# Kernel tuning notes

Measured on AMD Instinct MI355X. Metric: run time of the kernel, lower is better.

The kernel has to match this reference:

```python
import jax, jax.numpy as jnp
import numpy as np

BITS = (2, 4, 8)
GROUP = 4
EPS = 1e-5


def _ste_round(x):
    return x + jax.lax.stop_gradient(jnp.round(x) - x)


def _quant_act(x, b):
    s = float(2 ** b - 1)
    return _ste_round(jnp.clip(x, 0.0, 1.0) * s) / s


def _quant_weight(w, mean, std, b):
    # normalize by (mean, std) of the gating-selected channels, then b-bit uniform quant on [-1, 1]
    wn = jnp.clip((w - mean) / (std + EPS), -1.0, 1.0)
    s = float(2 ** b - 1)
    u = _ste_round((wn + 1.0) * 0.5 * s) / s
    return 2.0 * u - 1.0


def _mixed_qconv(x, w, w_mean, w_std, w_logits, a_logits):
    # bitwidth-selectable conv: softmax mixture over quantized weights / activations
    pw = jax.nn.softmax(w_logits)
    pa = jax.nn.softmax(a_logits)
    w_mix = sum(pw[i] * _quant_weight(w, w_mean, w_std, b) for i, b in enumerate(BITS))
    x_mix = sum(pa[i] * _quant_act(x, b) for i, b in enumerate(BITS))
    return jax.lax.conv_general_dilated(
        x_mix, w_mix, window_strides=(1, 1), padding='SAME',
        dimension_numbers=('NCHW', 'OIHW', 'NCHW'))


def _bn(x, g, b, m, v):
    inv = jax.lax.rsqrt(v + EPS)
    return (x - m[None, :, None, None]) * (g * inv)[None, :, None, None] + b[None, :, None, None]


def _masked_mean_std(w, mask):
    # mean/std over gate-selected filter slices; torch uses .data -> stop_gradient, unbiased std
    m = jnp.broadcast_to(mask, w.shape)
    cnt = jnp.sum(m)
    mean = jnp.sum(w * m) / cnt
    var = jnp.sum(m * (w - mean) ** 2) / (cnt - 1.0)
    return jax.lax.stop_gradient(mean), jax.lax.stop_gradient(jnp.sqrt(var))


def _indicator(w1, thr):
    n, c, h, wk = w1.shape
    fw = w1.reshape(n // GROUP, GROUP * c * h * wk)
    nf = fw / jnp.max(jnp.abs(fw))
    norm = jnp.sum(jnp.abs(nf), axis=1) / (GROUP * c * h * wk)  # [n_choices]
    soft = jax.nn.sigmoid(norm - thr)
    hard = (norm > thr).astype(w1.dtype)
    return hard - jax.lax.stop_gradient(soft) + soft  # STE indicator


def setup_inputs() -> dict:
    key = jax.random.key(0)
    ks = jax.random.split(key, 10)
    B, C, H, W = 64, 256, 32, 32
    return {
        'x': jax.random.normal(ks[0], (B, C, H, W), jnp.float32),
        'w1': jax.random.normal(ks[1], (C, C, 3, 3), jnp.float32) * 0.05,
        'w2': jax.random.normal(ks[2], (C, C, 3, 3), jnp.float32) * 0.05,
        'bn1_gamma': jnp.ones((C,), jnp.float32),
        'bn1_beta': jnp.zeros((C,), jnp.float32),
        'bn1_mean': jax.random.normal(ks[3], (C,), jnp.float32) * 0.1,
        'bn1_var': jax.random.uniform(ks[4], (C,), jnp.float32, 0.5, 1.5),
        'bn2_gamma': jnp.ones((C,), jnp.float32),
        'bn2_beta': jnp.zeros((C,), jnp.float32),
        'bn2_mean': jax.random.normal(ks[5], (C,), jnp.float32) * 0.1,
        'bn2_var': jax.random.uniform(ks[6], (C,), jnp.float32, 0.5, 1.5),
        'threshold': jnp.zeros((1,), jnp.float32),
        'w_logits1': jax.random.normal(ks[7], (3,), jnp.float32) * 0.1,
        'a_logits1': jax.random.normal(ks[8], (3,), jnp.float32) * 0.1,
        'w_logits2': jax.random.normal(ks[9], (3,), jnp.float32) * 0.1,
        'a_logits2': jnp.zeros((3,), jnp.float32),
    }


def reference(x, w1, w2, bn1_gamma, bn1_beta, bn1_mean, bn1_var,
              bn2_gamma, bn2_beta, bn2_mean, bn2_var, threshold,
              w_logits1, a_logits1, w_logits2, a_logits2):
    thr = threshold[0]
    ind = _indicator(w1, thr)                       # [n_choices]
    ind_ch = jnp.repeat(ind, GROUP)                 # [out_plane]
    gate_mask = jax.lax.stop_gradient((ind_ch > 0).astype(x.dtype))

    # both_preact path
    residual = x
    h = jax.nn.relu(_bn(x, bn1_gamma, bn1_beta, bn1_mean, bn1_var))
    m1, s1 = _masked_mean_std(w1, gate_mask[:, None, None, None])
    h = _mixed_qconv(h, w1, m1, s1, w_logits1, a_logits1)
    h = jax.nn.relu(_bn(h, bn2_gamma, bn2_beta, bn2_mean, bn2_var))
    m2, s2 = _masked_mean_std(w2, gate_mask[None, :, None, None])
    h = h * ind_ch[None, :, None, None]             # differentiable channel gating
    h = _mixed_qconv(h, w2, m2, s2, w_logits2, a_logits2)
    return h + residual
```

## Files before the change

kernel.cpp:

```cpp
#include <hip/hip_runtime.h>
#include <stdint.h>

#define EPSF 1e-5f

typedef _Float16 h8_t __attribute__((ext_vector_type(8)));
typedef float f4_t __attribute__((ext_vector_type(4)));

#define BB 64
#define CC 256
#define HH 32
#define WW 32
#define HP 34
#define WP 34
#define PADIMG (HP*WP*CC)
#define PADTOT (BB*PADIMG)

#define S_GSUM   0
#define S_GMAX   64
#define S_W1S    128
#define S_W1Q    192
#define S_W2S    256
#define S_W2Q    320
#define S_PA2    384
#define S_INDCH  400
#define S_BN2SC  656
#define S_BN2SH  912

#define OFF_STATS 0
#define OFF_A1    8192
#define OFF_A2    (OFF_A1 + PADTOT*2)
#define OFF_W1T   (OFF_A2 + PADTOT*2)
#define OFF_W2T   (OFF_W1T + 9*CC*CC*2)

__device__ __forceinline__ void async_load16(void* lds, const void* g) {
  __builtin_amdgcn_global_load_lds(
      reinterpret_cast<uint32_t __attribute__((address_space(1)))*>((uintptr_t)g),
      reinterpret_cast<uint32_t __attribute__((address_space(3)))*>((uint32_t)(uintptr_t)lds),
      16, 0, 0);
}

__device__ __forceinline__ float wave_sum(float v) {
  for (int o = 32; o; o >>= 1) v += __shfl_down(v, o);
  return v;
}
__device__ __forceinline__ float wave_max(float v) {
  for (int o = 32; o; o >>= 1) v = fmaxf(v, __shfl_down(v, o));
  return v;
}

__device__ __forceinline__ void softmax3(const float* l, float* out) {
  float m = fmaxf(fmaxf(l[0], l[1]), l[2]);
  float e0 = expf(l[0] - m), e1 = expf(l[1] - m), e2 = expf(l[2] - m);
  float inv = 1.f / (e0 + e1 + e2);
  out[0] = e0 * inv; out[1] = e1 * inv; out[2] = e2 * inv;
}

__device__ __forceinline__ float qmix_act(float v, float p0, float p1, float p2) {
  float cl = fminf(fmaxf(v, 0.f), 1.f);
  return p0 * (rintf(cl * 3.f) / 3.f) + p1 * (rintf(cl * 15.f) / 15.f)
       + p2 * (rintf(cl * 255.f) / 255.f);
}

__global__ void k_stats(const float* __restrict__ w1, const float* __restrict__ w2,
                        float* stats) {
  __shared__ float red[4][4];
  int bid = blockIdx.x, t = threadIdx.x;
  int lane = t & 63, w = t >> 6;
  if (bid < 64) {
    const float* p = w1 + bid * 9216;
    float sa = 0.f, s = 0.f, q = 0.f, mx = 0.f;
    for (int i = t; i < 9216; i += 256) {
      float v = p[i];
      float a = fabsf(v);
      sa += a; s += v; q += v * v; mx = fmaxf(mx, a);
    }
    sa = wave_sum(sa); s = wave_sum(s); q = wave_sum(q); mx = wave_max(mx);
    if (lane == 0) { red[w][0] = sa; red[w][1] = s; red[w][2] = q; red[w][3] = mx; }
    __syncthreads();
    if (t == 0) {
      float a = 0, b = 0, c = 0, d = 0;
      for (int k = 0; k < 4; ++k) {
        a += red[k][0]; b += red[k][1]; c += red[k][2]; d = fmaxf(d, red[k][3]);
      }
      stats[S_GSUM + bid] = a;
      stats[S_W1S + bid] = b;
      stats[S_W1Q + bid] = c;
      stats[S_GMAX + bid] = d;
    }
  } else {
    int g = bid - 64;
    const float* p = w2 + (size_t)t * 2304 + g * 36;
    float s = 0.f, q = 0.f;
#pragma unroll
    for (int i = 0; i < 36; ++i) { float v = p[i]; s += v; q += v * v; }
    s = wave_sum(s); q = wave_sum(q);
    if (lane == 0) { red[w][0] = s; red[w][1] = q; }
    __syncthreads();
    if (t == 0) {
      float a = 0, b = 0;
      for (int k = 0; k < 4; ++k) { a += red[k][0]; b += red[k][1]; }
      stats[S_W2S + g] = a;
      stats[S_W2Q + g] = b;
    }
  }
}

#define WPS 264
#define APR_STRIDE 264
__global__ void k_fused(const float* __restrict__ w1, const float* __restrict__ w2,
                        const float* __restrict__ xin, const float* __restrict__ thr_p,
                        const float* __restrict__ bn1g, const float* __restrict__ bn1b,
                        const float* __restrict__ bn1m, const float* __restrict__ bn1v,
                        const float* __restrict__ bn2g, const float* __restrict__ bn2b,
                        const float* __restrict__ bn2m, const float* __restrict__ bn2v,
                        const float* __restrict__ wl1, const float* __restrict__ al1,
                        const float* __restrict__ wl2, const float* __restrict__ al2,
                        float* __restrict__ stats,
                        _Float16* __restrict__ wt1, _Float16* __restrict__ wt2,
                        _Float16* __restrict__ a1, _Float16* __restrict__ a2) {
  int bid = blockIdx.x, t = threadIdx.x;

  if (bid == 0) {
    __shared__ float sind[64];
    if (t < 64) {
      float thr = thr_p[0];
      float mx = wave_max(stats[S_GMAX + t]);
      mx = __shfl(mx, 0);
      float norm = stats[S_GSUM + t] / mx / 9216.0f;
      float soft = 1.f / (1.f + expf(-(norm - thr)));
      float hard = (norm > thr) ? 1.f : 0.f;
      sind[t] = (hard - soft) + soft;
    }
    __syncthreads();
    stats[S_INDCH + t] = sind[t >> 2];
    float sc2 = bn2g[t] * (1.f / sqrtf(bn2v[t] + EPSF));
    stats[S_BN2SC + t] = sc2;
    stats[S_BN2SH + t] = bn2b[t] - bn2m[t] * sc2;
    if (t == 0) softmax3(al2, stats + S_PA2);
    return;
  }

  if (bid <= 512) {
    __shared__ __attribute__((aligned(16))) _Float16 lds[9 * WPS];
    __shared__ float sM, sSD, sP[3];
    int which = (bid - 1) >> 8, o = (bid - 1) & 255;
    if (t < 64) {
      float thr = thr_p[0];
      float mx = wave_max(stats[S_GMAX + t]);
      mx = __shfl(mx, 0);
      float norm = stats[S_GSUM + t] / mx / 9216.0f;
      float soft = 1.f / (1.f + expf(-(norm - thr)));
      float hard = (norm > thr) ? 1.f : 0.f;
      float iv = (hard - soft) + soft;
      float gate = (iv > 0.f) ? 1.f : 0.f;
      float ng = wave_sum(gate);
      float s = wave_sum(gate * stats[(which ? S_W2S : S_W1S) + t]);
      float q = wave_sum(gate * stats[(which ? S_W2Q : S_W1Q) + t]);
      if (t == 0) {
        float cnt = ng * 9216.0f;
        float m = s / cnt;
        float v = (q - cnt * m * m) / (cnt - 1.0f);
        sM = m; sSD = sqrtf(fmaxf(v, 0.f));
        softmax3(which ? wl2 : wl1, sP);
      }
    }
    __syncthreads();
    const float* w = (which ? w2 : w1) + (size_t)o * 2304;
    float mean = sM, sd = sSD + EPSF;
    float p0 = sP[0], p1 = sP[1], p2 = sP[2];
#pragma unroll
    for (int it = 0; it < 9; ++it) {
      int f = it * 256 + t;
      float v = w[f];
      float wn = fminf(fmaxf((v - mean) / sd, -1.f), 1.f);
      float u0 = rintf((wn + 1.f) * 0.5f * 3.f) / 3.f;
      float u1 = rintf((wn + 1.f) * 0.5f * 15.f) / 15.f;
      float u2 = rintf((wn + 1.f) * 0.5f * 255.f) / 255.f;
      float mix = p0 * (2.f * u0 - 1.f) + p1 * (2.f * u1 - 1.f) + p2 * (2.f * u2 - 1.f);
      int ci = f / 9;
      int e = f - 9 * ci;
      lds[e * WPS + ci] = (_Float16)mix;
    }
    __syncthreads();
    _Float16* dst0 = (which ? wt2 : wt1) + o * 256;
#pragma unroll
    for (int it = 0; it < 2; ++it) {
      int qid = it * 256 + t;
      if (qid < 288) {
        int e = qid >> 5, c8 = (qid & 31) * 8;
        *(h8_t*)(dst0 + e * 65536 + c8) = *(const h8_t*)(lds + e * WPS + c8);
      }
    }
    return;
  }

  int ab = bid - 513;
  if (ab >= BB * HH) {
    int b = ab - BB * HH;
    _Float16* img = (b >= BB ? a2 : a1) + (size_t)(b & 63) * PADIMG;
    uint64_t* u = (uint64_t*)img;
#pragma unroll
    for (int it = 0; it < 17; ++it) {
      int idx = it * 256 + t;
      int r33 = (idx >= 2176);
      u[(size_t)(r33 ? 33 * WP * 64 : 0) + (idx - (r33 ? 2176 : 0))] = 0ull;
    }
#pragma unroll
    for (int it = 0; it < 16; ++it) {
      int idx = it * 256 + t;
      int p = idx >> 6;
      int y = 1 + (p >> 1), x = (p & 1) ? 33 : 0;
      u[(size_t)(y * WP + x) * 64 + (idx & 63)] = 0ull;
    }
    return;
  }

  __shared__ __attribute__((aligned(16))) _Float16 lds[32 * APR_STRIDE];
  __shared__ float sBsc[256], sBsh[256], sPa[3];
  {
    float sc1 = bn1g[t] * (1.f / sqrtf(bn1v[t] + EPSF));
    sBsc[t] = sc1;
    sBsh[t] = bn1b[t] - bn1m[t] * sc1;
    if (t == 0) softmax3(al1, sPa);
  }
  __syncthreads();
  int n = ab >> 5, y = ab & 31;
  int x4 = (t & 7) * 4, c0 = t >> 3;
  float pa0 = sPa[0], pa1 = sPa[1], pa2 = sPa[2];
#pragma unroll
  for (int it = 0; it < 8; ++it) {
    int c = it * 32 + c0;
    const float* src = xin + ((size_t)(n * CC + c) * HH + y) * WW + x4;
    float4 v = *(const float4*)src;
    float sc = sBsc[c], sh = sBsh[c];
#pragma unroll
    for (int k = 0; k < 4; ++k) {
      float q = qmix_act((&v.x)[k] * sc + sh, pa0, pa1, pa2);
      lds[(x4 + k) * APR_STRIDE + c] = (_Float16)q;
    }
  }
  __syncthreads();
  _Float16* orow = a1 + ((size_t)(n * HP + (y + 1)) * WP + 1) * CC;
#pragma unroll
  for (int it = 0; it < 4; ++it) {
    int qid = it * 256 + t;
    int xx = qid >> 5, c8 = (qid & 31) * 8;
    *(h8_t*)(orow + xx * CC + c8) = *(const h8_t*)(lds + xx * APR_STRIDE + c8);
  }
}

template <bool SW>
__global__ __launch_bounds__(256) void k_conv(
    const _Float16* __restrict__ act,
    const _Float16* __restrict__ wts,
    const float* __restrict__ stats,
    _Float16* __restrict__ a2out,
    const float* __restrict__ resid,
    float* __restrict__ out) {
  __shared__ __attribute__((aligned(16))) _Float16 As[128 * 64];
  __shared__ __attribute__((aligned(16))) _Float16 Ws[128 * 64];
  const int tid = threadIdx.x;
  const int lane = tid & 63, wid = tid >> 6;
  const int xcd = blockIdx.x & 7;
  const int j = blockIdx.x >> 3;
  const int blk_co = j >> 6;
  const int blk_m = xcd * 64 + (j & 63);

  const int srow = wid * 8 + (lane >> 3);
  const int g = (lane & 7) ^ (lane >> 3);
  int abase[4], wbase[4];
#pragma unroll
  for (int q = 0; q < 4; ++q) {
    int r = q * 32 + srow;
    int m = blk_m * 128 + r;
    int n = m >> 10, y = (m >> 5) & 31, x = m & 31;
    abase[q] = ((n * HP + y) * WP + x) * CC + g * 8;
    wbase[q] = (blk_co * 128 + r) * CC + g * 8;
  }

  const int wr = wid >> 1, wc = wid & 1;

  f4_t acc[4][4];
  const f4_t z4 = {0.f, 0.f, 0.f, 0.f};
#pragma unroll
  for (int i = 0; i < 4; ++i)
#pragma unroll
    for (int j2 = 0; j2 < 4; ++j2) acc[i][j2] = z4;

  int raoff[4], rboff[4];
#pragma unroll
  for (int i = 0; i < 4; ++i) {
    int ra = wr * 64 + i * 16 + (lane & 15);
    int sa = (lane >> 4) ^ (lane & 7);
    raoff[i] = ra * 64 + sa * 8;
    int rb = wc * 64 + i * 16 + (lane & 15);
    rboff[i] = rb * 64 + sa * 8;
  }

#pragma unroll 1
  for (int kc = 0; kc < 4; ++kc) {
    const int kb = kc * 64;
#pragma unroll
    for (int e = 0; e < 9; ++e) {
      const int kh = e / 3, kw = e - 3 * kh;
      const int ao = (kh * WP + kw) * CC + kb;
      const int wo = e * CC * CC + kb;
      __syncthreads();
#pragma unroll
      for (int q = 0; q < 4; ++q) {
        async_load16(As + (q * 32 + wid * 8) * 64, act + abase[q] + ao);
        async_load16(Ws + (q * 32 + wid * 8) * 64, wts + wbase[q] + wo);
      }
      __syncthreads();
      const _Float16* aT = SW ? Ws : As;
      const _Float16* bT = SW ? As : Ws;
#pragma unroll
      for (int kk = 0; kk < 2; ++kk) {
        h8_t fa[4], fb[4];
#pragma unroll
        for (int i = 0; i < 4; ++i) {
          fa[i] = *(const h8_t*)(aT + (raoff[i] ^ (kk * 32)));
          fb[i] = *(const h8_t*)(bT + (rboff[i] ^ (kk * 32)));
        }
#pragma unroll
        for (int i = 0; i < 4; ++i)
#pragma unroll
          for (int j2 = 0; j2 < 4; ++j2)
            acc[i][j2] = __builtin_amdgcn_mfma_f32_16x16x32_f16(fa[i], fb[j2], acc[i][j2], 0, 0, 0);
      }
    }
  }

  const int quad = lane >> 4;
  const int cq = lane & 15;
  if (!SW) {
    const float pa0 = stats[S_PA2], pa1 = stats[S_PA2 + 1], pa2 = stats[S_PA2 + 2];
#pragma unroll
    for (int j2 = 0; j2 < 4; ++j2) {
      const int co = blk_co * 128 + wc * 64 + j2 * 16 + cq;
      const float sc = stats[S_BN2SC + co];
      const float sh = stats[S_BN2SH + co];
      const float ic = stats[S_INDCH + co];
#pragma unroll
      for (int i = 0; i < 4; ++i) {
        const int mbase = blk_m * 128 + wr * 64 + i * 16 + quad * 4;
#pragma unroll
        for (int rg = 0; rg < 4; ++rg) {
          const int m = mbase + rg;
          const int n = m >> 10, y = (m >> 5) & 31, x = m & 31;
          float h = fmaxf(acc[i][j2][rg] * sc + sh, 0.f) * ic;
          float q = qmix_act(h, pa0, pa1, pa2);
          a2out[((size_t)(n * HP + y + 1) * WP + (x + 1)) * CC + co] = (_Float16)q;
        }
      }
    }
  } else {
#pragma unroll
    for (int j2 = 0; j2 < 4; ++j2) {
      const int m = blk_m * 128 + wc * 64 + j2 * 16 + cq;
      const int n = m >> 10, y = (m >> 5) & 31, x = m & 31;
#pragma unroll
      for (int i = 0; i < 4; ++i) {
        const int cobase = blk_co * 128 + wr * 64 + i * 16 + quad * 4;
#pragma unroll
        for (int rg = 0; rg < 4; ++rg) {
          const int co = cobase + rg;
          const int idx = ((n * CC + co) << 10) + (y << 5) + x;
          out[idx] = acc[i][j2][rg] + resid[idx];
        }
      }
    }
  }
}

extern "C" void kernel_launch(void* const* d_in, const int* in_sizes, int n_in,
                              void* d_out, int out_size, void* d_ws, size_t ws_size,
                              hipStream_t stream) {
  const float* x    = (const float*)d_in[0];
  const float* w1   = (const float*)d_in[1];
  const float* w2   = (const float*)d_in[2];
  const float* bn1g = (const float*)d_in[3];
  const float* bn1b = (const float*)d_in[4];
  const float* bn1m = (const float*)d_in[5];
  const float* bn1v = (const float*)d_in[6];
  const float* bn2g = (const float*)d_in[7];
  const float* bn2b = (const float*)d_in[8];
  const float* bn2m = (const float*)d_in[9];
  const float* bn2v = (const float*)d_in[10];
  const float* thr  = (const float*)d_in[11];
  const float* wl1  = (const float*)d_in[12];
  const float* al1  = (const float*)d_in[13];
  const float* wl2  = (const float*)d_in[14];
  const float* al2  = (const float*)d_in[15];

  char* ws = (char*)d_ws;
  float* stats = (float*)(ws + OFF_STATS);
  _Float16* a1 = (_Float16*)(ws + OFF_A1);
  _Float16* a2 = (_Float16*)(ws + OFF_A2);
  _Float16* wt1 = (_Float16*)(ws + OFF_W1T);
  _Float16* wt2 = (_Float16*)(ws + OFF_W2T);
  float* out = (float*)d_out;

  k_stats<<<128, 256, 0, stream>>>(w1, w2, stats);
  k_fused<<<1 + 512 + BB * HH + 128, 256, 0, stream>>>(
      w1, w2, x, thr, bn1g, bn1b, bn1m, bn1v, bn2g, bn2b, bn2m, bn2v,
      wl1, al1, wl2, al2, stats, wt1, wt2, a1, a2);
  k_conv<false><<<1024, 256, 0, stream>>>(a1, wt1, stats, a2, nullptr, nullptr);
  k_conv<true><<<1024, 256, 0, stream>>>(a2, wt2, stats, nullptr, x, out);
}
```

Baseline: 345.3 us.

## Stage halo activation tile once per K-chunk and double-buffer weight tiles

The conv kernel now loads a 6x34-pixel halo tile of activations into LDS once per 64-channel chunk and reuses it across all 9 filter taps. Before, it reloaded a shifted 128-row tile for every tap. Weight tiles are double-buffered, with the next tap's weights prefetched asynchronously under partial vmcnt waits and raw s_barrier, which overlaps loads with MFMA work. The cost is more LDS per block (halo plus two weight buffers), which may lower occupancy. There is also an exposed stall at each K-chunk boundary where the activation tile is reloaded without overlap.

```diff
diff --git a/kernel.cpp b/kernel.cpp
--- a/kernel.cpp
+++ b/kernel.cpp
@@ -38,6 +38,9 @@
       reinterpret_cast<uint32_t __attribute__((address_space(3)))*>((uint32_t)(uintptr_t)lds),
       16, 0, 0);
 }
+
+#define WAITV4() asm volatile("s_waitcnt vmcnt(4)" ::: "memory")
+#define WAITV0() asm volatile("s_waitcnt vmcnt(0)" ::: "memory")
 
 __device__ __forceinline__ float wave_sum(float v) {
   for (int o = 32; o; o >>= 1) v += __shfl_down(v, o);
@@ -257,8 +260,8 @@
     _Float16* __restrict__ a2out,
     const float* __restrict__ resid,
     float* __restrict__ out) {
-  __shared__ __attribute__((aligned(16))) _Float16 As[128 * 64];
-  __shared__ __attribute__((aligned(16))) _Float16 Ws[128 * 64];
+  __shared__ __attribute__((aligned(16))) _Float16 AT[204 * 64];
+  __shared__ __attribute__((aligned(16))) _Float16 WB[2 * 128 * 64];
   const int tid = threadIdx.x;
   const int lane = tid & 63, wid = tid >> 6;
   const int xcd = blockIdx.x & 7;
@@ -268,17 +271,28 @@
 
   const int srow = wid * 8 + (lane >> 3);
   const int g = (lane & 7) ^ (lane >> 3);
-  int abase[4], wbase[4];
-#pragma unroll
-  for (int q = 0; q < 4; ++q) {
-    int r = q * 32 + srow;
-    int m = blk_m * 128 + r;
-    int n = m >> 10, y = (m >> 5) & 31, x = m & 31;
-    abase[q] = ((n * HP + y) * WP + x) * CC + g * 8;
-    wbase[q] = (blk_co * 128 + r) * CC + g * 8;
-  }
+  int wbase[4];
+#pragma unroll
+  for (int q = 0; q < 4; ++q)
+    wbase[q] = (blk_co * 128 + q * 32 + srow) * CC + g * 8;
+
+  const int n0 = blk_m >> 3;
+  const int y0 = (blk_m & 7) * 4;
+  const _Float16* actbase = act + (size_t)(n0 * HP + y0) * WP * CC;
 
   const int wr = wid >> 1, wc = wid & 1;
+  const int mrow = (SW ? wc : wr) * 64;
+  const int wrow = (SW ? wr : wc) * 64;
+  const int ksl = lane >> 4;
+
+  int trbase[4], woff[4];
+#pragma unroll
+  for (int i = 0; i < 4; ++i) {
+    int r = mrow + i * 16 + (lane & 15);
+    trbase[i] = (r >> 5) * 34 + (r & 31);
+    int rb = wrow + i * 16 + (lane & 15);
+    woff[i] = rb * 64 + ((ksl ^ (lane & 7)) * 8);
+  }
 
   f4_t acc[4][4];
   const f4_t z4 = {0.f, 0.f, 0.f, 0.f};
@@ -287,48 +301,83 @@
 #pragma unroll
     for (int j2 = 0; j2 < 4; ++j2) acc[i][j2] = z4;
 
-  int raoff[4], rboff[4];
-#pragma unroll
-  for (int i = 0; i < 4; ++i) {
-    int ra = wr * 64 + i * 16 + (lane & 15);
-    int sa = (lane >> 4) ^ (lane & 7);
-    raoff[i] = ra * 64 + sa * 8;
-    int rb = wc * 64 + i * 16 + (lane & 15);
-    rboff[i] = rb * 64 + sa * 8;
-  }
-
+  auto stageW = [&](int kcn, int en, int nb_) {
+    const int wo = en * (CC * CC) + kcn * 64;
+    _Float16* dst = WB + nb_ * (128 * 64);
+#pragma unroll
+    for (int q = 0; q < 4; ++q)
+      async_load16(dst + (q * 32 + wid * 8) * 64, wts + wbase[q] + wo);
+  };
+  auto stageA = [&](int kcn) {
+    const int kb = kcn * 64;
+#pragma unroll
+    for (int it = 0; it < 6; ++it) {
+      int l = it * 256 + tid;
+      int tr = l >> 3, gg = l & 7;
+      int yl = tr / 34, px = tr - yl * 34;
+      async_load16(AT + l * 8,
+                   actbase + ((size_t)yl * WP + px) * CC + kb + ((gg ^ (tr & 7)) * 8));
+    }
+    if (tid < 96) {
+      int l = 1536 + tid;
+      int tr = l >> 3, gg = l & 7;
+      int yl = tr / 34, px = tr - yl * 34;
+      async_load16(AT + l * 8,
+                   actbase + ((size_t)yl * WP + px) * CC + kb + ((gg ^ (tr & 7)) * 8));
+    }
+  };
+
+  stageA(0);
+  stageW(0, 0, 0);
+  int nb = 0;
 #pragma unroll 1
   for (int kc = 0; kc < 4; ++kc) {
-    const int kb = kc * 64;
 #pragma unroll
     for (int e = 0; e < 9; ++e) {
-      const int kh = e / 3, kw = e - 3 * kh;
-      const int ao = (kh * WP + kw) * CC + kb;
-      const int wo = e * CC * CC + kb;
-      __syncthreads();
-#pragma unroll
-      for (int q = 0; q < 4; ++q) {
-        async_load16(As + (q * 32 + wid * 8) * 64, act + abase[q] + ao);
-        async_load16(Ws + (q * 32 + wid * 8) * 64, wts + wbase[q] + wo);
-      }
-      __syncthreads();
-      const _Float16* aT = SW ? Ws : As;
-      const _Float16* bT = SW ? As : Ws;
+      if (e < 8) {
+        stageW(kc, e + 1, nb ^ 1);
+        WAITV4();
+      } else if (kc < 3) {
+        stageW(kc + 1, 0, nb ^ 1);
+        WAITV4();
+      } else {
+        WAITV0();
+      }
+      __builtin_amdgcn_s_barrier();
+      asm volatile("" ::: "memory");
+      __builtin_amdgcn_sched_barrier(0);
+
+      const int de = (e / 3) * 34 + (e % 3);
+      const _Float16* WBc = WB + nb * (128 * 64);
+      __builtin_amdgcn_s_setprio(1);
+      int aoff[4];
+#pragma unroll
+      for (int i = 0; i < 4; ++i) {
+        int tr = trbase[i] + de;
+        aoff[i] = tr * 64 + ((ksl ^ (tr & 7)) * 8);
+      }
 #pragma unroll
       for (int kk = 0; kk < 2; ++kk) {
-        h8_t fa[4], fb[4];
+        h8_t fa[4], fw[4];
 #pragma unroll
         for (int i = 0; i < 4; ++i) {
-          fa[i] = *(const h8_t*)(aT + (raoff[i] ^ (kk * 32)));
-          fb[i] = *(const h8_t*)(bT + (rboff[i] ^ (kk * 32)));
+          fa[i] = *(const h8_t*)(AT + (aoff[i] ^ (kk * 32)));
+          fw[i] = *(const h8_t*)(WBc + (woff[i] ^ (kk * 32)));
         }
 #pragma unroll
         for (int i = 0; i < 4; ++i)
 #pragma unroll
           for (int j2 = 0; j2 < 4; ++j2)
-            acc[i][j2] = __builtin_amdgcn_mfma_f32_16x16x32_f16(fa[i], fb[j2], acc[i][j2], 0, 0, 0);
-      }
-    }
+            acc[i][j2] = __builtin_amdgcn_mfma_f32_16x16x32_f16(
+                SW ? fw[i] : fa[i], SW ? fa[j2] : fw[j2], acc[i][j2], 0, 0, 0);
+      }
+      __builtin_amdgcn_s_setprio(0);
+      asm volatile("" ::: "memory");
+      __builtin_amdgcn_s_barrier();
+      __builtin_amdgcn_sched_barrier(0);
+      nb ^= 1;
+    }
+    if (kc < 3) stageA(kc + 1);
   }
 
   const int quad = lane >> 4;
```

Measured after the change: 362.1 us. 4.9% more time.
